# Optimization experiments

Hardware: AMD Instinct MI355X
Metric: run time of the kernel (lower is better)

The kernel has to match this reference:

```python
import jax, jax.numpy as jnp
import numpy as np

H = 16  # head_num
NEG = -1000000.0


def setup_inputs() -> dict:
    key = jax.random.key(0)
    k1, k2, k3 = jax.random.split(key, 3)
    B, S, D = 4, 2048, 1024
    d = D // H
    x = jax.random.normal(k1, (B, S, D), dtype=jnp.float32)
    mask = jax.random.randint(k2, (B, S), 0, 2, dtype=jnp.int32)
    W = jax.random.normal(k3, (d, d), dtype=jnp.float32) * (1.0 / np.sqrt(d))
    b = jnp.zeros((d,), dtype=jnp.float32)
    return {"x": x, "mask": mask, "W": W, "b": b}


def reference(x, mask, W, b):
    B, S, D = x.shape
    d = D // H
    # [B,S,D] -> [B,H,S,d]
    x_h = jnp.transpose(x.reshape(B, S, H, d), (0, 2, 1, 3))
    # shared Dense(d) produces q and k (and the unused v) with the SAME weights
    q = x_h @ W + b
    k = x_h @ W + b
    # scores, scaled by d (not sqrt(d)) as in the source
    qkt = jnp.einsum('bhqd,bhkd->bhqk', q, k) / d
    # additive mask: (1-mask)*-1e6, broadcast [B,1,S,1] over query rows
    m = (1.0 - mask.astype(x.dtype)) * NEG
    qkt = qkt + m[:, None, :, None]
    attn = jax.nn.softmax(qkt, axis=-1)
    # second matmul uses x_h (not v), per the source
    a = jnp.einsum('bhqk,bhkd->bhqd', attn, x_h)
    # direct reshape (no head transpose back), per the source
    return a.reshape(B, S, D)
```

## Files before the change

### kernel.cpp

```cpp
#include <hip/hip_runtime.h>
#include <math.h>


#define S_LEN   2048
#define D_MODEL 1024
#define HD      64
#define NHEAD   16
#define QT      256
#define KT2     64
#define NKT     (S_LEN / KT2)

typedef __bf16 bf16;
typedef __bf16 bf16x8 __attribute__((ext_vector_type(8)));
typedef __bf16 bf16x4 __attribute__((ext_vector_type(4)));
typedef __bf16 bf16x2 __attribute__((ext_vector_type(2)));
typedef float  floatx16 __attribute__((ext_vector_type(16)));
typedef unsigned int u32;
typedef u32 u32x4 __attribute__((ext_vector_type(4)));

#define SCALE 0.02254211001389005324f

__device__ __forceinline__ floatx16 mfma32(bf16x8 a, bf16x8 b, floatx16 c) {
    return __builtin_amdgcn_mfma_f32_32x32x16_bf16(a, b, c, 0, 0, 0);
}

__device__ __forceinline__ void ldsdma16(void* lds_base, const void* gsrc) {
    __builtin_amdgcn_global_load_lds(
        (const __attribute__((address_space(1))) u32*)gsrc,
        (__attribute__((address_space(3))) u32*)lds_base, 16, 0, 0);
}

__device__ __forceinline__ u32 pack2(bf16 lo, bf16 hi) {
    bf16x2 p = { lo, hi };
    return __builtin_bit_cast(u32, p);
}

__device__ __forceinline__ u32 cvtpk(float lo, float hi) {
    u32 r;
    asm("v_cvt_pk_bf16_f32 %0, %1, %2" : "=v"(r) : "v"(lo), "v"(hi));
    return r;
}
__device__ __forceinline__ void swap32(u32& x, u32& y) {
    asm("v_permlane32_swap_b32 %0, %1" : "+v"(x), "+v"(y));
}

__global__ __launch_bounds__(256)
void prex_kernel(const float* __restrict__ x, const float* __restrict__ W,
                 const float* __restrict__ bvec,
                 bf16* __restrict__ Xb, bf16* __restrict__ XT,
                 float* __restrict__ Uout, bf16* __restrict__ Mout) {
    __shared__ __align__(16) char smem[16896];
    u32*   sT = (u32*)smem;
    float* Wp = (float*)smem;
    float* bs = (float*)(smem + 16640);

    const int tid = threadIdx.x;
    const int st = blockIdx.x, h = blockIdx.y, b = blockIdx.z;

    if (st == 16) {
        if (h != 0 || b != 0) return;
        for (int i = tid; i < 4096; i += 256) Wp[(i >> 6) * 65 + (i & 63)] = W[i];
        if (tid < 64) bs[tid] = bvec[tid];
        __syncthreads();
        for (int e = tid; e < 4096; e += 256) {
            int i = e >> 6, j = e & 63;
            float acc = 0.f;
            #pragma unroll 8
            for (int c = 0; c < 64; ++c) acc += Wp[i * 65 + c] * Wp[j * 65 + c];
            Mout[e] = (bf16)(acc * SCALE);
        }
        if (tid < 64) {
            float acc = 0.f;
            #pragma unroll 8
            for (int c = 0; c < 64; ++c) acc += Wp[tid * 65 + c] * bs[c];
            Uout[tid] = acc * SCALE;
        }
        return;
    }

    const int bh = b * NHEAD + h;
    const float* xbh = x + (size_t)b * S_LEN * D_MODEL + (size_t)st * 128 * D_MODEL + h * HD;
    bf16* Xbbh = Xb + ((size_t)bh * S_LEN + st * 128) * HD;

    const int t  = tid & 15;
    const int rp = tid >> 4;
    const int c4 = t * 4;

    #pragma unroll
    for (int it = 0; it < 4; ++it) {
        const int r0 = it * 32 + rp * 2;
        float4 v0 = *(const float4*)(xbh + (size_t)r0 * D_MODEL + c4);
        float4 v1 = *(const float4*)(xbh + (size_t)(r0 + 1) * D_MODEL + c4);
        bf16 a0 = (bf16)v0.x, a1 = (bf16)v0.y, a2 = (bf16)v0.z, a3 = (bf16)v0.w;
        bf16 b0 = (bf16)v1.x, b1 = (bf16)v1.y, b2 = (bf16)v1.z, b3 = (bf16)v1.w;
        bf16x4 p0 = { a0, a1, a2, a3 }, p1 = { b0, b1, b2, b3 };
        *(bf16x4*)(Xbbh + (size_t)r0 * HD + c4)       = p0;
        *(bf16x4*)(Xbbh + (size_t)(r0 + 1) * HD + c4) = p1;
        const int w = it * 16 + rp;
        sT[(c4 + 0) * 65 + w] = pack2(a0, b0);
        sT[(c4 + 1) * 65 + w] = pack2(a1, b1);
        sT[(c4 + 2) * 65 + w] = pack2(a2, b2);
        sT[(c4 + 3) * 65 + w] = pack2(a3, b3);
    }
    __syncthreads();

    bf16* XTbh = XT + (size_t)bh * HD * S_LEN + (size_t)st * 128;
    #pragma unroll
    for (int i = 0; i < 4; ++i) {
        const int c  = i * 256 + tid;
        const int dd = c >> 4;
        const int wg = (c & 15) * 4;
        u32x4 qv = { sT[dd * 65 + wg],     sT[dd * 65 + wg + 1],
                     sT[dd * 65 + wg + 2], sT[dd * 65 + wg + 3] };
        *(u32x4*)((char*)(XTbh + (size_t)dd * S_LEN) + (size_t)wg * 4) = qv;
    }
}

__global__ __launch_bounds__(256, 2)
void attn_kernel(const bf16* __restrict__ Xb, const bf16* __restrict__ XT,
                 const bf16* __restrict__ Mw, const float* __restrict__ Uv,
                 float* __restrict__ out) {
    __shared__ bf16  sXk [2 * KT2 * HD];
    __shared__ bf16  sXkT[2 * HD * KT2];
    __shared__ float sL[4][64];

    const int tid  = threadIdx.x;
    const int wave = tid >> 6, lane = tid & 63;
    const int hi   = lane >> 5, q32 = lane & 31;
    const int wbase = wave * 64;
    const int bh = blockIdx.x, qt = blockIdx.y;
    const int q0 = qt * QT;

    const char* Xbh  = (const char*)(Xb + (size_t)bh * S_LEN * HD);
    const char* XTbh = (const char*)(XT + (size_t)bh * HD * S_LEN);

    const floatx16 z16 = {0,0,0,0, 0,0,0,0, 0,0,0,0, 0,0,0,0};

    bf16x8 Tfrag[2][4];
    {
        floatx16 Tacc[2][2];
        #pragma unroll
        for (int mt = 0; mt < 2; ++mt)
            #pragma unroll
            for (int ddt = 0; ddt < 2; ++ddt) Tacc[mt][ddt] = z16;

        #pragma unroll
        for (int kc = 0; kc < 4; ++kc) {
            bf16x8 am[2], xq[2];
            #pragma unroll
            for (int ddt = 0; ddt < 2; ++ddt)
                am[ddt] = *(const bf16x8*)(Mw + (ddt * 32 + q32) * 64 + kc * 16 + hi * 8);
            #pragma unroll
            for (int mt = 0; mt < 2; ++mt)
                xq[mt] = *(const bf16x8*)(Xbh +
                    (size_t)(q0 + wbase + mt * 32 + q32) * 128 + kc * 32 + hi * 16);
            #pragma unroll
            for (int mt = 0; mt < 2; ++mt)
                #pragma unroll
                for (int ddt = 0; ddt < 2; ++ddt)
                    Tacc[mt][ddt] = mfma32(am[ddt], xq[mt], Tacc[mt][ddt]);
        }
        #pragma unroll
        for (int ddt = 0; ddt < 2; ++ddt)
            #pragma unroll
            for (int r = 0; r < 16; ++r) {
                float uu = Uv[ddt * 32 + 8 * (r >> 2) + 4 * hi + (r & 3)];
                #pragma unroll
                for (int mt = 0; mt < 2; ++mt) Tacc[mt][ddt][r] += uu;
            }
        #pragma unroll
        for (int mt = 0; mt < 2; ++mt)
            #pragma unroll
            for (int kc = 0; kc < 4; ++kc) {
                const int ddt = kc >> 1, a4 = 8 * (kc & 1);
                u32 X  = cvtpk(Tacc[mt][ddt][a4 + 0], Tacc[mt][ddt][a4 + 1]);
                u32 Y  = cvtpk(Tacc[mt][ddt][a4 + 4], Tacc[mt][ddt][a4 + 5]);
                swap32(X, Y);
                u32 X2 = cvtpk(Tacc[mt][ddt][a4 + 2], Tacc[mt][ddt][a4 + 3]);
                u32 Y2 = cvtpk(Tacc[mt][ddt][a4 + 6], Tacc[mt][ddt][a4 + 7]);
                swap32(X2, Y2);
                u32x4 w = { X, X2, Y, Y2 };
                Tfrag[mt][kc] = __builtin_bit_cast(bf16x8, w);
            }
    }

    auto stage = [&](int kt, int par) {
        const int k0 = kt * KT2;
        #pragma unroll
        for (int j = 0; j < 2; ++j) {
            int s = wave * 16 + j * 8 + (lane >> 3);
            const char* g = Xbh + (size_t)(k0 + s) * 128 + (((lane & 7) ^ (s & 7)) << 4);
            ldsdma16((char*)sXk + par * 8192 + (wave * 16 + j * 8) * 128, g);
        }
        #pragma unroll
        for (int j = 0; j < 2; ++j) {
            int dd = wave * 16 + j * 8 + (lane >> 3);
            const char* g = XTbh + (size_t)dd * 4096 + (size_t)k0 * 2 + (((lane & 7) ^ (dd & 7)) << 4);
            ldsdma16((char*)sXkT + par * 8192 + (wave * 16 + j * 8) * 128, g);
        }
    };

    floatx16 Oacc[2][2];
    float l_run[2] = {0.f, 0.f};
    #pragma unroll
    for (int mt = 0; mt < 2; ++mt)
        #pragma unroll
        for (int nt = 0; nt < 2; ++nt) Oacc[mt][nt] = z16;

    stage(0, 0);

    auto body = [&](int kt, const int par) {
        __syncthreads();
        if (kt + 1 < NKT) stage(kt + 1, par ^ 1);

        const char* xkb = (const char*)sXk + par * 8192;
        floatx16 Sacc[2][2];
        #pragma unroll
        for (int mt = 0; mt < 2; ++mt)
            #pragma unroll
            for (int k32t = 0; k32t < 2; ++k32t) Sacc[mt][k32t] = z16;
        __builtin_amdgcn_s_setprio(1);
        #pragma unroll
        for (int kc = 0; kc < 4; ++kc) {
            bf16x8 ak[2];
            #pragma unroll
            for (int k32t = 0; k32t < 2; ++k32t)
                ak[k32t] = *(const bf16x8*)(xkb + (k32t * 32 + q32) * 128 +
                                            (((2 * kc + hi) ^ (q32 & 7)) << 4));
            #pragma unroll
            for (int mt = 0; mt < 2; ++mt)
                #pragma unroll
                for (int k32t = 0; k32t < 2; ++k32t)
                    Sacc[mt][k32t] = mfma32(ak[k32t], Tfrag[mt][kc], Sacc[mt][k32t]);
        }
        __builtin_amdgcn_s_setprio(0);

        #pragma unroll
        for (int mt = 0; mt < 2; ++mt)
            #pragma unroll
            for (int k32t = 0; k32t < 2; ++k32t)
                #pragma unroll
                for (int r = 0; r < 16; ++r) {
                    float pe = __builtin_amdgcn_exp2f(Sacc[mt][k32t][r]);
                    Sacc[mt][k32t][r] = pe;
                    l_run[mt] += pe;
                }

        const char* xktb = (const char*)sXkT + par * 8192;
        #pragma unroll
        for (int s = 0; s < 4; ++s) {
            const int k32t = s >> 1, a4 = 8 * (s & 1);
            bf16x8 pa[2];
            #pragma unroll
            for (int mt = 0; mt < 2; ++mt) {
                u32 X  = cvtpk(Sacc[mt][k32t][a4 + 0], Sacc[mt][k32t][a4 + 1]);
                u32 Y  = cvtpk(Sacc[mt][k32t][a4 + 4], Sacc[mt][k32t][a4 + 5]);
                swap32(X, Y);
                u32 X2 = cvtpk(Sacc[mt][k32t][a4 + 2], Sacc[mt][k32t][a4 + 3]);
                u32 Y2 = cvtpk(Sacc[mt][k32t][a4 + 6], Sacc[mt][k32t][a4 + 7]);
                swap32(X2, Y2);
                u32x4 w = { X, X2, Y, Y2 };
                pa[mt] = __builtin_bit_cast(bf16x8, w);
            }
            __builtin_amdgcn_s_setprio(1);
            #pragma unroll
            for (int nt = 0; nt < 2; ++nt) {
                const int dd = nt * 32 + q32;
                bf16x8 bb = *(const bf16x8*)(xktb + dd * 128 +
                                             (((2 * s + hi) ^ (q32 & 7)) << 4));
                #pragma unroll
                for (int mt = 0; mt < 2; ++mt)
                    Oacc[mt][nt] = mfma32(pa[mt], bb, Oacc[mt][nt]);
            }
            __builtin_amdgcn_s_setprio(0);
        }
    };

    for (int kt = 0; kt < NKT; kt += 2) {
        body(kt, 0);
        body(kt + 1, 1);
    }

    #pragma unroll
    for (int mt = 0; mt < 2; ++mt) {
        float lt = l_run[mt] + __shfl_xor(l_run[mt], 32);
        if (hi == 0) sL[wave][mt * 32 + q32] = 1.0f / lt;
    }
    __syncthreads();

    float* outb = out + ((size_t)bh * S_LEN + q0) * HD;
    #pragma unroll
    for (int mt = 0; mt < 2; ++mt)
        #pragma unroll
        for (int r = 0; r < 16; ++r) {
            const int qlocal = 8 * (r >> 2) + 4 * hi + (r & 3);
            const float rl = sL[wave][mt * 32 + qlocal];
            const int qrow = wbase + mt * 32 + qlocal;
            #pragma unroll
            for (int nt = 0; nt < 2; ++nt)
                outb[(size_t)qrow * HD + nt * 32 + q32] = Oacc[mt][nt][r] * rl;
        }
}

extern "C" void kernel_launch(void* const* d_in, const int* in_sizes, int n_in,
                              void* d_out, int out_size, void* d_ws, size_t ws_size,
                              hipStream_t stream) {
    const float* x    = (const float*)d_in[0];
    const float* W    = (const float*)d_in[2];
    const float* bvec = (const float*)d_in[3];

    bf16*  Mws = (bf16*)d_ws;
    float* Uws = (float*)((char*)d_ws + 8192);
    bf16*  Xbws = (bf16*)((char*)d_ws + 540672);
    bf16*  XTws = (bf16*)((char*)d_ws + 17317888);

    prex_kernel<<<dim3(17, 16, 4), dim3(256), 0, stream>>>(x, W, bvec,
                                                           Xbws, XTws, Uws, Mws);
    attn_kernel<<<dim3(64, 8, 1),  dim3(256), 0, stream>>>(Xbws, XTws, Mws, Uws,
                                                           (float*)d_out);
}
```

Baseline: 167.0 us.

## Software-pipeline QK^T MFMA with softmax/PV using 4-stage LDS ring buffer

Replaces the double-buffered K tile loop with a four-slot LDS ring and two prefetched stages, and splits each iteration into an S-issue phase and a finish phase (exp, convert, PV). The S MFMAs for tile t+1 are issued before the exp/PV work of tile t, so matrix and vector work can overlap. Explicit vmcnt waits and raw s_barrier replace __syncthreads. LDS use grows to about 65KB per block, which may limit the two-blocks-per-CU occupancy and adds register pressure from holding two score accumulator sets.

```diff
diff --git a/kernel.cpp b/kernel.cpp
--- a/kernel.cpp
+++ b/kernel.cpp
@@ -43,6 +43,12 @@
 __device__ __forceinline__ void swap32(u32& x, u32& y) {
     asm("v_permlane32_swap_b32 %0, %1" : "+v"(x), "+v"(y));
 }
+
+#define VMCNT_WAIT(n) do { \
+    asm volatile("s_waitcnt vmcnt(" #n ")" ::: "memory"); \
+    __builtin_amdgcn_sched_barrier(0); } while (0)
+#define BARRIER() do { __builtin_amdgcn_s_barrier(); \
+    __builtin_amdgcn_sched_barrier(0); } while (0)
 
 __global__ __launch_bounds__(256)
 void prex_kernel(const float* __restrict__ x, const float* __restrict__ W,
@@ -120,9 +126,8 @@
 void attn_kernel(const bf16* __restrict__ Xb, const bf16* __restrict__ XT,
                  const bf16* __restrict__ Mw, const float* __restrict__ Uv,
                  float* __restrict__ out) {
-    __shared__ bf16  sXk [2 * KT2 * HD];
-    __shared__ bf16  sXkT[2 * HD * KT2];
-    __shared__ float sL[4][64];
+    __shared__ __align__(16) char smem[4 * 16384 + 1024];
+    float (*sL)[64] = (float(*)[64])(smem + 65536);
 
     const int tid  = threadIdx.x;
     const int wave = tid >> 6, lane = tid & 63;
@@ -184,19 +189,20 @@
             }
     }
 
-    auto stage = [&](int kt, int par) {
+    auto stage = [&](int kt, int idx) {
+        char* base = smem + idx * 16384;
         const int k0 = kt * KT2;
         #pragma unroll
         for (int j = 0; j < 2; ++j) {
             int s = wave * 16 + j * 8 + (lane >> 3);
             const char* g = Xbh + (size_t)(k0 + s) * 128 + (((lane & 7) ^ (s & 7)) << 4);
-            ldsdma16((char*)sXk + par * 8192 + (wave * 16 + j * 8) * 128, g);
+            ldsdma16(base + (wave * 16 + j * 8) * 128, g);
         }
         #pragma unroll
         for (int j = 0; j < 2; ++j) {
             int dd = wave * 16 + j * 8 + (lane >> 3);
             const char* g = XTbh + (size_t)dd * 4096 + (size_t)k0 * 2 + (((lane & 7) ^ (dd & 7)) << 4);
-            ldsdma16((char*)sXkT + par * 8192 + (wave * 16 + j * 8) * 128, g);
+            ldsdma16(base + 8192 + (wave * 16 + j * 8) * 128, g);
         }
     };
 
@@ -207,18 +213,8 @@
         #pragma unroll
         for (int nt = 0; nt < 2; ++nt) Oacc[mt][nt] = z16;
 
-    stage(0, 0);
-
-    auto body = [&](int kt, const int par) {
-        __syncthreads();
-        if (kt + 1 < NKT) stage(kt + 1, par ^ 1);
-
-        const char* xkb = (const char*)sXk + par * 8192;
-        floatx16 Sacc[2][2];
-        #pragma unroll
-        for (int mt = 0; mt < 2; ++mt)
-            #pragma unroll
-            for (int k32t = 0; k32t < 2; ++k32t) Sacc[mt][k32t] = z16;
+    auto Sissue = [&](floatx16 (&S)[2][2], int idx) {
+        const char* xkb = (const char*)smem + idx * 16384;
         __builtin_amdgcn_s_setprio(1);
         #pragma unroll
         for (int kc = 0; kc < 4; ++kc) {
@@ -231,33 +227,35 @@
             for (int mt = 0; mt < 2; ++mt)
                 #pragma unroll
                 for (int k32t = 0; k32t < 2; ++k32t)
-                    Sacc[mt][k32t] = mfma32(ak[k32t], Tfrag[mt][kc], Sacc[mt][k32t]);
+                    S[mt][k32t] = mfma32(ak[k32t], Tfrag[mt][kc],
+                                         kc == 0 ? z16 : S[mt][k32t]);
         }
         __builtin_amdgcn_s_setprio(0);
-
+    };
+
+    auto fin = [&](floatx16 (&S)[2][2], int idx) {
         #pragma unroll
         for (int mt = 0; mt < 2; ++mt)
             #pragma unroll
             for (int k32t = 0; k32t < 2; ++k32t)
                 #pragma unroll
                 for (int r = 0; r < 16; ++r) {
-                    float pe = __builtin_amdgcn_exp2f(Sacc[mt][k32t][r]);
-                    Sacc[mt][k32t][r] = pe;
+                    float pe = __builtin_amdgcn_exp2f(S[mt][k32t][r]);
+                    S[mt][k32t][r] = pe;
                     l_run[mt] += pe;
                 }
-
-        const char* xktb = (const char*)sXkT + par * 8192;
+        const char* xktb = (const char*)smem + idx * 16384 + 8192;
         #pragma unroll
         for (int s = 0; s < 4; ++s) {
             const int k32t = s >> 1, a4 = 8 * (s & 1);
             bf16x8 pa[2];
             #pragma unroll
             for (int mt = 0; mt < 2; ++mt) {
-                u32 X  = cvtpk(Sacc[mt][k32t][a4 + 0], Sacc[mt][k32t][a4 + 1]);
-                u32 Y  = cvtpk(Sacc[mt][k32t][a4 + 4], Sacc[mt][k32t][a4 + 5]);
+                u32 X  = cvtpk(S[mt][k32t][a4 + 0], S[mt][k32t][a4 + 1]);
+                u32 Y  = cvtpk(S[mt][k32t][a4 + 4], S[mt][k32t][a4 + 5]);
                 swap32(X, Y);
-                u32 X2 = cvtpk(Sacc[mt][k32t][a4 + 2], Sacc[mt][k32t][a4 + 3]);
-                u32 Y2 = cvtpk(Sacc[mt][k32t][a4 + 6], Sacc[mt][k32t][a4 + 7]);
+                u32 X2 = cvtpk(S[mt][k32t][a4 + 2], S[mt][k32t][a4 + 3]);
+                u32 Y2 = cvtpk(S[mt][k32t][a4 + 6], S[mt][k32t][a4 + 7]);
                 swap32(X2, Y2);
                 u32x4 w = { X, X2, Y, Y2 };
                 pa[mt] = __builtin_bit_cast(bf16x8, w);
@@ -276,10 +274,29 @@
         }
     };
 
-    for (int kt = 0; kt < NKT; kt += 2) {
-        body(kt, 0);
-        body(kt + 1, 1);
-    }
+    floatx16 SA[2][2], SB[2][2];
+
+    stage(0, 0);
+    stage(1, 1);
+    VMCNT_WAIT(4);
+    BARRIER();
+    Sissue(SA, 0);
+
+    for (int t = 1; t < NKT; t += 2) {
+        if (t + 1 < NKT) { stage(t + 1, (t + 1) & 3); VMCNT_WAIT(4); }
+        else            { VMCNT_WAIT(0); }
+        BARRIER();
+        Sissue(SB, t & 3);
+        fin(SA, (t - 1) & 3);
+        if (t + 1 < NKT) {
+            if (t + 2 < NKT) { stage(t + 2, (t + 2) & 3); VMCNT_WAIT(4); }
+            else             { VMCNT_WAIT(0); }
+            BARRIER();
+            Sissue(SA, (t + 1) & 3);
+            fin(SB, t & 3);
+        }
+    }
+    fin(SB, (NKT - 1) & 3);
 
     #pragma unroll
     for (int mt = 0; mt < 2; ++mt) {
```

Measured after the change: 299.1 us. 79.1% more time.

## Split attention query tile across eight waves with one 32-row tile each

Applied to the files above, without the earlier changes.

The attention block grows from 4 to 8 waves, and each wave now handles 32 query rows instead of 64. Per-wave accumulators, T fragments and S tiles are halved, which lowers register pressure and raises wave occupancy (launch bounds 512,4). Each wave now stages a single 8-row slice of K/K^T into LDS. The cost is that every wave reads each staged LDS K tile for only half as many MFMAs, so LDS traffic per FLOP doubles and barrier overhead is shared across more waves.

```diff
diff --git a/kernel.cpp b/kernel.cpp
--- a/kernel.cpp
+++ b/kernel.cpp
@@ -116,18 +116,18 @@
     }
 }
 
-__global__ __launch_bounds__(256, 2)
+__global__ __launch_bounds__(512, 4)
 void attn_kernel(const bf16* __restrict__ Xb, const bf16* __restrict__ XT,
                  const bf16* __restrict__ Mw, const float* __restrict__ Uv,
                  float* __restrict__ out) {
     __shared__ bf16  sXk [2 * KT2 * HD];
     __shared__ bf16  sXkT[2 * HD * KT2];
-    __shared__ float sL[4][64];
+    __shared__ float sL[8][32];
 
     const int tid  = threadIdx.x;
     const int wave = tid >> 6, lane = tid & 63;
     const int hi   = lane >> 5, q32 = lane & 31;
-    const int wbase = wave * 64;
+    const int wbase = wave * 32;
     const int bh = blockIdx.x, qt = blockIdx.y;
     const int q0 = qt * QT;
 
@@ -136,76 +136,61 @@
 
     const floatx16 z16 = {0,0,0,0, 0,0,0,0, 0,0,0,0, 0,0,0,0};
 
-    bf16x8 Tfrag[2][4];
+    bf16x8 Tfrag[4];
     {
-        floatx16 Tacc[2][2];
-        #pragma unroll
-        for (int mt = 0; mt < 2; ++mt)
-            #pragma unroll
-            for (int ddt = 0; ddt < 2; ++ddt) Tacc[mt][ddt] = z16;
+        floatx16 Tacc[2];
+        #pragma unroll
+        for (int ddt = 0; ddt < 2; ++ddt) Tacc[ddt] = z16;
 
         #pragma unroll
         for (int kc = 0; kc < 4; ++kc) {
-            bf16x8 am[2], xq[2];
+            bf16x8 am[2];
             #pragma unroll
             for (int ddt = 0; ddt < 2; ++ddt)
                 am[ddt] = *(const bf16x8*)(Mw + (ddt * 32 + q32) * 64 + kc * 16 + hi * 8);
-            #pragma unroll
-            for (int mt = 0; mt < 2; ++mt)
-                xq[mt] = *(const bf16x8*)(Xbh +
-                    (size_t)(q0 + wbase + mt * 32 + q32) * 128 + kc * 32 + hi * 16);
-            #pragma unroll
-            for (int mt = 0; mt < 2; ++mt)
-                #pragma unroll
-                for (int ddt = 0; ddt < 2; ++ddt)
-                    Tacc[mt][ddt] = mfma32(am[ddt], xq[mt], Tacc[mt][ddt]);
+            bf16x8 xq = *(const bf16x8*)(Xbh +
+                (size_t)(q0 + wbase + q32) * 128 + kc * 32 + hi * 16);
+            #pragma unroll
+            for (int ddt = 0; ddt < 2; ++ddt)
+                Tacc[ddt] = mfma32(am[ddt], xq, Tacc[ddt]);
         }
         #pragma unroll
         for (int ddt = 0; ddt < 2; ++ddt)
             #pragma unroll
-            for (int r = 0; r < 16; ++r) {
-                float uu = Uv[ddt * 32 + 8 * (r >> 2) + 4 * hi + (r & 3)];
-                #pragma unroll
-                for (int mt = 0; mt < 2; ++mt) Tacc[mt][ddt][r] += uu;
-            }
-        #pragma unroll
-        for (int mt = 0; mt < 2; ++mt)
-            #pragma unroll
-            for (int kc = 0; kc < 4; ++kc) {
-                const int ddt = kc >> 1, a4 = 8 * (kc & 1);
-                u32 X  = cvtpk(Tacc[mt][ddt][a4 + 0], Tacc[mt][ddt][a4 + 1]);
-                u32 Y  = cvtpk(Tacc[mt][ddt][a4 + 4], Tacc[mt][ddt][a4 + 5]);
-                swap32(X, Y);
-                u32 X2 = cvtpk(Tacc[mt][ddt][a4 + 2], Tacc[mt][ddt][a4 + 3]);
-                u32 Y2 = cvtpk(Tacc[mt][ddt][a4 + 6], Tacc[mt][ddt][a4 + 7]);
-                swap32(X2, Y2);
-                u32x4 w = { X, X2, Y, Y2 };
-                Tfrag[mt][kc] = __builtin_bit_cast(bf16x8, w);
-            }
+            for (int r = 0; r < 16; ++r)
+                Tacc[ddt][r] += Uv[ddt * 32 + 8 * (r >> 2) + 4 * hi + (r & 3)];
+        #pragma unroll
+        for (int kc = 0; kc < 4; ++kc) {
+            const int ddt = kc >> 1, a4 = 8 * (kc & 1);
+            u32 X  = cvtpk(Tacc[ddt][a4 + 0], Tacc[ddt][a4 + 1]);
+            u32 Y  = cvtpk(Tacc[ddt][a4 + 4], Tacc[ddt][a4 + 5]);
+            swap32(X, Y);
+            u32 X2 = cvtpk(Tacc[ddt][a4 + 2], Tacc[ddt][a4 + 3]);
+            u32 Y2 = cvtpk(Tacc[ddt][a4 + 6], Tacc[ddt][a4 + 7]);
+            swap32(X2, Y2);
+            u32x4 w = { X, X2, Y, Y2 };
+            Tfrag[kc] = __builtin_bit_cast(bf16x8, w);
+        }
     }
 
     auto stage = [&](int kt, int par) {
         const int k0 = kt * KT2;
-        #pragma unroll
-        for (int j = 0; j < 2; ++j) {
-            int s = wave * 16 + j * 8 + (lane >> 3);
+        {
+            int s = wave * 8 + (lane >> 3);
             const char* g = Xbh + (size_t)(k0 + s) * 128 + (((lane & 7) ^ (s & 7)) << 4);
-            ldsdma16((char*)sXk + par * 8192 + (wave * 16 + j * 8) * 128, g);
-        }
-        #pragma unroll
-        for (int j = 0; j < 2; ++j) {
-            int dd = wave * 16 + j * 8 + (lane >> 3);
+            ldsdma16((char*)sXk + par * 8192 + wave * 1024, g);
+        }
+        {
+            int dd = wave * 8 + (lane >> 3);
             const char* g = XTbh + (size_t)dd * 4096 + (size_t)k0 * 2 + (((lane & 7) ^ (dd & 7)) << 4);
-            ldsdma16((char*)sXkT + par * 8192 + (wave * 16 + j * 8) * 128, g);
+            ldsdma16((char*)sXkT + par * 8192 + wave * 1024, g);
         }
     };
 
-    floatx16 Oacc[2][2];
-    float l_run[2] = {0.f, 0.f};
-    #pragma unroll
-    for (int mt = 0; mt < 2; ++mt)
-        #pragma unroll
-        for (int nt = 0; nt < 2; ++nt) Oacc[mt][nt] = z16;
+    floatx16 Oacc[2];
+    float l_run = 0.f;
+    #pragma unroll
+    for (int nt = 0; nt < 2; ++nt) Oacc[nt] = z16;
 
     stage(0, 0);
 
@@ -214,11 +199,9 @@
         if (kt + 1 < NKT) stage(kt + 1, par ^ 1);
 
         const char* xkb = (const char*)sXk + par * 8192;
-        floatx16 Sacc[2][2];
-        #pragma unroll
-        for (int mt = 0; mt < 2; ++mt)
-            #pragma unroll
-            for (int k32t = 0; k32t < 2; ++k32t) Sacc[mt][k32t] = z16;
+        floatx16 Sacc[2];
+        #pragma unroll
+        for (int k32t = 0; k32t < 2; ++k32t) Sacc[k32t] = z16;
         __builtin_amdgcn_s_setprio(1);
         #pragma unroll
         for (int kc = 0; kc < 4; ++kc) {
@@ -228,49 +211,39 @@
                 ak[k32t] = *(const bf16x8*)(xkb + (k32t * 32 + q32) * 128 +
                                             (((2 * kc + hi) ^ (q32 & 7)) << 4));
             #pragma unroll
-            for (int mt = 0; mt < 2; ++mt)
-                #pragma unroll
-                for (int k32t = 0; k32t < 2; ++k32t)
-                    Sacc[mt][k32t] = mfma32(ak[k32t], Tfrag[mt][kc], Sacc[mt][k32t]);
+            for (int k32t = 0; k32t < 2; ++k32t)
+                Sacc[k32t] = mfma32(ak[k32t], Tfrag[kc], Sacc[k32t]);
         }
         __builtin_amdgcn_s_setprio(0);
 
         #pragma unroll
-        for (int mt = 0; mt < 2; ++mt)
-            #pragma unroll
-            for (int k32t = 0; k32t < 2; ++k32t)
-                #pragma unroll
-                for (int r = 0; r < 16; ++r) {
-                    float pe = __builtin_amdgcn_exp2f(Sacc[mt][k32t][r]);
-                    Sacc[mt][k32t][r] = pe;
-                    l_run[mt] += pe;
-                }
+        for (int k32t = 0; k32t < 2; ++k32t)
+            #pragma unroll
+            for (int r = 0; r < 16; ++r) {
+                float pe = __builtin_amdgcn_exp2f(Sacc[k32t][r]);
+                Sacc[k32t][r] = pe;
+                l_run += pe;
+            }
 
         const char* xktb = (const char*)sXkT + par * 8192;
         #pragma unroll
         for (int s = 0; s < 4; ++s) {
             const int k32t = s >> 1, a4 = 8 * (s & 1);
-            bf16x8 pa[2];
-            #pragma unroll
-            for (int mt = 0; mt < 2; ++mt) {
-                u32 X  = cvtpk(Sacc[mt][k32t][a4 + 0], Sacc[mt][k32t][a4 + 1]);
-                u32 Y  = cvtpk(Sacc[mt][k32t][a4 + 4], Sacc[mt][k32t][a4 + 5]);
-                swap32(X, Y);
-                u32 X2 = cvtpk(Sacc[mt][k32t][a4 + 2], Sacc[mt][k32t][a4 + 3]);
-                u32 Y2 = cvtpk(Sacc[mt][k32t][a4 + 6], Sacc[mt][k32t][a4 + 7]);
-                swap32(X2, Y2);
-                u32x4 w = { X, X2, Y, Y2 };
-                pa[mt] = __builtin_bit_cast(bf16x8, w);
-            }
+            u32 X  = cvtpk(Sacc[k32t][a4 + 0], Sacc[k32t][a4 + 1]);
+            u32 Y  = cvtpk(Sacc[k32t][a4 + 4], Sacc[k32t][a4 + 5]);
+            swap32(X, Y);
+            u32 X2 = cvtpk(Sacc[k32t][a4 + 2], Sacc[k32t][a4 + 3]);
+            u32 Y2 = cvtpk(Sacc[k32t][a4 + 6], Sacc[k32t][a4 + 7]);
+            swap32(X2, Y2);
+            u32x4 w = { X, X2, Y, Y2 };
+            bf16x8 pa = __builtin_bit_cast(bf16x8, w);
             __builtin_amdgcn_s_setprio(1);
             #pragma unroll
             for (int nt = 0; nt < 2; ++nt) {
                 const int dd = nt * 32 + q32;
                 bf16x8 bb = *(const bf16x8*)(xktb + dd * 128 +
                                              (((2 * s + hi) ^ (q32 & 7)) << 4));
-                #pragma unroll
-                for (int mt = 0; mt < 2; ++mt)
-                    Oacc[mt][nt] = mfma32(pa[mt], bb, Oacc[mt][nt]);
+                Oacc[nt] = mfma32(pa, bb, Oacc[nt]);
             }
             __builtin_amdgcn_s_setprio(0);
         }
@@ -281,25 +254,22 @@
         body(kt + 1, 1);
     }
 
-    #pragma unroll
-    for (int mt = 0; mt < 2; ++mt) {
-        float lt = l_run[mt] + __shfl_xor(l_run[mt], 32);
-        if (hi == 0) sL[wave][mt * 32 + q32] = 1.0f / lt;
+    {
+        float lt = l_run + __shfl_xor(l_run, 32);
+        if (hi == 0) sL[wave][q32] = 1.0f / lt;
     }
     __syncthreads();
 
     float* outb = out + ((size_t)bh * S_LEN + q0) * HD;
     #pragma unroll
-    for (int mt = 0; mt < 2; ++mt)
-        #pragma unroll
-        for (int r = 0; r < 16; ++r) {
-            const int qlocal = 8 * (r >> 2) + 4 * hi + (r & 3);
-            const float rl = sL[wave][mt * 32 + qlocal];
-            const int qrow = wbase + mt * 32 + qlocal;
-            #pragma unroll
-            for (int nt = 0; nt < 2; ++nt)
-                outb[(size_t)qrow * HD + nt * 32 + q32] = Oacc[mt][nt][r] * rl;
-        }
+    for (int r = 0; r < 16; ++r) {
+        const int qlocal = 8 * (r >> 2) + 4 * hi + (r & 3);
+        const float rl = sL[wave][qlocal];
+        const int qrow = wbase + qlocal;
+        #pragma unroll
+        for (int nt = 0; nt < 2; ++nt)
+            outb[(size_t)qrow * HD + nt * 32 + q32] = Oacc[nt][r] * rl;
+    }
 }
 
 extern "C" void kernel_launch(void* const* d_in, const int* in_sizes, int n_in,
@@ -316,6 +286,6 @@
 
     prex_kernel<<<dim3(17, 16, 4), dim3(256), 0, stream>>>(x, W, bvec,
                                                            Xbws, XTws, Uws, Mws);
-    attn_kernel<<<dim3(64, 8, 1),  dim3(256), 0, stream>>>(Xbws, XTws, Mws, Uws,
+    attn_kernel<<<dim3(64, 8, 1),  dim3(512), 0, stream>>>(Xbws, XTws, Mws, Uws,
                                                            (float*)d_out);
 }
```

New measurement: 171.9 us. 1.03x slower.
